# Kernel optimization log

Hardware: AMD Instinct MI355X
Metric: run time of the kernel (lower is better)

Reference implementation:

```python
import jax, jax.numpy as jnp
import numpy as np

B, L, D = 16384, 32, 128
DIAG_LEN, PROC_LEN, MED_LEN = 100000, 50000, 1000


def setup_inputs() -> dict:
    key = jax.random.key(0)
    ks = jax.random.split(key, 12)
    inp = {
        "diag_codes": jax.random.randint(ks[0], (B, L), 0, DIAG_LEN),
        "proc_codes": jax.random.randint(ks[1], (B, L), 0, PROC_LEN),
        "prev_diag_codes": jax.random.randint(ks[2], (B, L), 0, DIAG_LEN),
        "prev_proc_codes": jax.random.randint(ks[3], (B, L), 0, PROC_LEN),
        # learned parameters (torch Linear convention: W[out,in], y = x @ W.T + b)
        "diag_emb": jax.random.normal(ks[4], (DIAG_LEN, D), jnp.float32) * 0.02,
        "proc_emb": jax.random.normal(ks[5], (PROC_LEN, D), jnp.float32) * 0.02,
        "W1": jax.random.normal(ks[6], (D, 2 * D), jnp.float32) * 0.02,
        "b1": jnp.zeros((D,), jnp.float32),
        "W2": jax.random.normal(ks[7], (256, 2 * D), jnp.float32) * 0.02,
        "b2": jnp.zeros((256,), jnp.float32),
        "W3": jax.random.normal(ks[8], (MED_LEN, 256), jnp.float32) * 0.02,
        "b3": jnp.zeros((MED_LEN,), jnp.float32),
    }
    return inp


def _bag_sum(table, idx):
    # EmbeddingBag('sum'): gather [B,L,D] then reduce over codes -> [B,D]
    return jnp.take(table, idx, axis=0).sum(axis=1)


def reference(diag_codes, proc_codes, prev_diag_codes, prev_proc_codes,
              diag_emb, proc_emb, W1, b1, W2, b2, W3, b3):
    emb_d = _bag_sum(diag_emb, diag_codes)            # [B,128]
    emb_p = _bag_sum(proc_emb, proc_codes)            # [B,128]
    prev_d = _bag_sum(diag_emb, prev_diag_codes)      # [B,128]
    prev_p = _bag_sum(proc_emb, prev_proc_codes)      # [B,128]

    # health_net = Linear(256->128) + Dropout (identity in eval mode)
    cur = jnp.concatenate([emb_d, emb_p], axis=1) @ W1.T + b1     # [B,128]
    prev = jnp.concatenate([prev_d, prev_p], axis=1) @ W1.T + b1  # [B,128]

    rep = jnp.concatenate([cur, prev], axis=1)        # [B,256]
    h = jax.nn.relu(rep @ W2.T + b2)                  # [B,256]
    return jax.nn.sigmoid(h @ W3.T + b3)              # [B,med_len]
```

## Files before the change

### kernel.cpp

```cpp
#include <hip/hip_runtime.h>
#include <hip/hip_bf16.h>
#include <math.h>

#define NB 16384
#define MED 1000
#define MD 100000
#define MP 50000
#define TDBLK 782
#define TPBLK 391

typedef __bf16 bf16x8 __attribute__((ext_vector_type(8)));
typedef float  f32x4  __attribute__((ext_vector_type(4)));
typedef unsigned short u16;
typedef unsigned int   u32;

__device__ __forceinline__ u16 f2bf(float f) {
    union { float f; u32 u; } v; v.f = f;
    u32 r = v.u + 0x7fffu + ((v.u >> 16) & 1u);
    return (u16)(r >> 16);
}
__device__ __forceinline__ float bflo(u32 u) { union { u32 u; float f; } v; v.u = u << 16;          return v.f; }
__device__ __forceinline__ float bfhi(u32 u) { union { u32 u; float f; } v; v.u = u & 0xffff0000u; return v.f; }

__global__ __launch_bounds__(256) void convert_kernel(
    const float* __restrict__ W1, const float* __restrict__ W2,
    const float* __restrict__ W3,
    u16* __restrict__ W1b, u16* __restrict__ W2b, u16* __restrict__ W3b)
{
    int i = blockIdx.x * 256 + threadIdx.x;
    if (i < 32768) { W1b[i] = f2bf(W1[i]); return; }
    i -= 32768;
    if (i < 65536) { W2b[i] = f2bf(W2[i]); return; }
    i -= 65536;
    if (i < 262144) W3b[i] = (i < MED * 256) ? f2bf(W3[i]) : (u16)0;
}

__global__ __launch_bounds__(256) void transform_kernel(
    const float* __restrict__ Ed, const float* __restrict__ Ep,
    const u16* __restrict__ W1b, u16* __restrict__ Td, u16* __restrict__ Tp)
{
    int blk = blockIdx.x;
    const float* E; u16* T; int M, koff;
    if (blk < TDBLK) { E = Ed; T = Td; M = MD; koff = 0; }
    else             { blk -= TDBLK; E = Ep; T = Tp; M = MP; koff = 128; }

    const int wave = threadIdx.x >> 6, lane = threadIdx.x & 63;
    const int quad = lane >> 4, l16 = lane & 15;
    const int m0 = blk * 128 + wave * 32 + l16;
    const float* aP0 = E + (size_t)min(m0,      M - 1) * 128 + quad * 8;
    const float* aP1 = E + (size_t)min(m0 + 16, M - 1) * 128 + quad * 8;
    const u16*   wP  = W1b + (size_t)l16 * 256 + koff + quad * 8;

    f32x4 acc[2][8];
    #pragma unroll
    for (int mt = 0; mt < 2; ++mt)
        #pragma unroll
        for (int nt = 0; nt < 8; ++nt) acc[mt][nt] = (f32x4){0.f, 0.f, 0.f, 0.f};

    #pragma unroll
    for (int ks = 0; ks < 4; ++ks) {
        union { bf16x8 v; u16 s[8]; } a0, a1;
        const float4 f0 = *(const float4*)(aP0 + ks * 32);
        const float4 f1 = *(const float4*)(aP0 + ks * 32 + 4);
        const float4 g0 = *(const float4*)(aP1 + ks * 32);
        const float4 g1 = *(const float4*)(aP1 + ks * 32 + 4);
        a0.s[0]=f2bf(f0.x); a0.s[1]=f2bf(f0.y); a0.s[2]=f2bf(f0.z); a0.s[3]=f2bf(f0.w);
        a0.s[4]=f2bf(f1.x); a0.s[5]=f2bf(f1.y); a0.s[6]=f2bf(f1.z); a0.s[7]=f2bf(f1.w);
        a1.s[0]=f2bf(g0.x); a1.s[1]=f2bf(g0.y); a1.s[2]=f2bf(g0.z); a1.s[3]=f2bf(g0.w);
        a1.s[4]=f2bf(g1.x); a1.s[5]=f2bf(g1.y); a1.s[6]=f2bf(g1.z); a1.s[7]=f2bf(g1.w);
        #pragma unroll
        for (int nt = 0; nt < 8; ++nt) {
            const bf16x8 b = *(const bf16x8*)(wP + nt * 16 * 256 + ks * 32);
            acc[0][nt] = __builtin_amdgcn_mfma_f32_16x16x32_bf16(a0.v, b, acc[0][nt], 0, 0, 0);
            acc[1][nt] = __builtin_amdgcn_mfma_f32_16x16x32_bf16(a1.v, b, acc[1][nt], 0, 0, 0);
        }
    }

    #pragma unroll
    for (int mt = 0; mt < 2; ++mt) {
        const int rb = blk * 128 + wave * 32 + mt * 16 + quad * 4;
        #pragma unroll
        for (int nt = 0; nt < 8; ++nt) {
            const int col = nt * 16 + l16;
            #pragma unroll
            for (int r = 0; r < 4; ++r) {
                const int row = rb + r;
                if (row < M) T[(size_t)row * 128 + col] = f2bf(acc[mt][nt][r]);
            }
        }
    }
}

__global__ __launch_bounds__(256) void gather_rep(
    const int* __restrict__ diag, const int* __restrict__ proc,
    const int* __restrict__ pdiag, const int* __restrict__ pproc,
    const u16* __restrict__ Td, const u16* __restrict__ Tp,
    const float* __restrict__ b1, u16* __restrict__ rep)
{
    __shared__ int   sidx[528];
    __shared__ float sred[128][8];
    const int t = threadIdx.x;

    for (int i = t; i < 512; i += 256) {
        const int s = i >> 7, bg = (i >> 5) & 3, l = i & 31;
        const int* cp = (bg == 0) ? diag : (bg == 1) ? proc : (bg == 2) ? pdiag : pproc;
        sidx[s * 132 + bg * 33 + l] = cp[(blockIdx.x * 4 + s) * 32 + l];
    }
    __syncthreads();

    const int sub = t >> 6, bag = (t >> 4) & 3, lc = t & 15;
    const u16* tbl = (bag & 1) ? Tp : Td;
    const int* myidx = &sidx[sub * 132 + bag * 33];

    float s0=0,s1=0,s2=0,s3=0,s4=0,s5=0,s6=0,s7=0;
    uint4 va[8], vb[8];
    #pragma unroll
    for (int j = 0; j < 8; ++j)
        va[j] = *(const uint4*)(tbl + (size_t)myidx[j] * 128 + lc * 8);
    #pragma unroll
    for (int j = 0; j < 8; ++j)
        vb[j] = *(const uint4*)(tbl + (size_t)myidx[8 + j] * 128 + lc * 8);

#define CONSUME(V) do { \
    _Pragma("unroll") \
    for (int j = 0; j < 8; ++j) { \
        s0 += bflo(V[j].x); s1 += bfhi(V[j].x); \
        s2 += bflo(V[j].y); s3 += bfhi(V[j].y); \
        s4 += bflo(V[j].z); s5 += bfhi(V[j].z); \
        s6 += bflo(V[j].w); s7 += bfhi(V[j].w); \
    } } while (0)

    {
        uint4 tmp[8];
        #pragma unroll
        for (int j = 0; j < 8; ++j)
            tmp[j] = *(const uint4*)(tbl + (size_t)myidx[16 + j] * 128 + lc * 8);
        CONSUME(va);
        #pragma unroll
        for (int j = 0; j < 8; ++j) va[j] = tmp[j];
    }
    {
        uint4 tmp[8];
        #pragma unroll
        for (int j = 0; j < 8; ++j)
            tmp[j] = *(const uint4*)(tbl + (size_t)myidx[24 + j] * 128 + lc * 8);
        CONSUME(vb);
        #pragma unroll
        for (int j = 0; j < 8; ++j) vb[j] = tmp[j];
    }
    CONSUME(va);
    CONSUME(vb);
#undef CONSUME

    const int oid = sub * 32 + (bag >> 1) * 16 + lc;
    if (bag & 1) {
        *(float4*)&sred[oid][0] = make_float4(s0, s1, s2, s3);
        *(float4*)&sred[oid][4] = make_float4(s4, s5, s6, s7);
    }
    __syncthreads();
    if (!(bag & 1)) {
        const float4 p0 = *(const float4*)&sred[oid][0];
        const float4 p1 = *(const float4*)&sred[oid][4];
        const float4 c0 = *(const float4*)(b1 + lc * 8);
        const float4 c1 = *(const float4*)(b1 + lc * 8 + 4);
        s0 += p0.x + c0.x; s1 += p0.y + c0.y; s2 += p0.z + c0.z; s3 += p0.w + c0.w;
        s4 += p1.x + c1.x; s5 += p1.y + c1.y; s6 += p1.z + c1.z; s7 += p1.w + c1.w;
        uint4 o;
        o.x = (u32)f2bf(s0) | ((u32)f2bf(s1) << 16);
        o.y = (u32)f2bf(s2) | ((u32)f2bf(s3) << 16);
        o.z = (u32)f2bf(s4) | ((u32)f2bf(s5) << 16);
        o.w = (u32)f2bf(s6) | ((u32)f2bf(s7) << 16);
        const int b = blockIdx.x * 4 + sub;
        *(uint4*)(rep + (size_t)b * 256 + (bag >> 1) * 128 + lc * 8) = o;
    }
}

__global__ __launch_bounds__(256) void gemm23(
    const u16* __restrict__ rep, const u16* __restrict__ W2b,
    const float* __restrict__ b2, const u16* __restrict__ W3b,
    const float* __restrict__ b3, float* __restrict__ out)
{
    __shared__ u16 hs[32][264];
    const int wave = threadIdx.x >> 6, lane = threadIdx.x & 63;
    const int quad = lane >> 4, l16 = lane & 15;
    const int mBase = blockIdx.x * 32;

    {
        const int mrow = mBase + (wave & 1) * 16 + l16;
        const int ncol0 = (wave >> 1) * 128;
        const u16* aP = rep + (size_t)mrow * 256 + quad * 8;
        bf16x8 a[8];
        #pragma unroll
        for (int ks = 0; ks < 8; ++ks) a[ks] = *(const bf16x8*)(aP + ks * 32);

        #pragma unroll
        for (int nt = 0; nt < 8; ++nt) {
            const int col = ncol0 + nt * 16 + l16;
            const u16* wP = W2b + (size_t)col * 256 + quad * 8;
            f32x4 acc = {0.f, 0.f, 0.f, 0.f};
            #pragma unroll
            for (int ks = 0; ks < 8; ++ks) {
                const bf16x8 b = *(const bf16x8*)(wP + ks * 32);
                acc = __builtin_amdgcn_mfma_f32_16x16x32_bf16(a[ks], b, acc, 0, 0, 0);
            }
            const float bv = b2[col];
            #pragma unroll
            for (int r = 0; r < 4; ++r) {
                float v = acc[r] + bv;
                v = v > 0.f ? v : 0.f;
                hs[(wave & 1) * 16 + quad * 4 + r][col] = f2bf(v);
            }
        }
    }
    __syncthreads();

    const int colW = wave * 256;
    #pragma unroll
    for (int nc = 0; nc < 4; ++nc) {
        f32x4 acc[2][4];
        #pragma unroll
        for (int mt = 0; mt < 2; ++mt)
            #pragma unroll
            for (int nti = 0; nti < 4; ++nti) acc[mt][nti] = (f32x4){0.f,0.f,0.f,0.f};

        #pragma unroll
        for (int ks = 0; ks < 8; ++ks) {
            bf16x8 af[2];
            #pragma unroll
            for (int mt = 0; mt < 2; ++mt)
                af[mt] = *(const bf16x8*)&hs[mt * 16 + l16][quad * 8 + ks * 32];
            #pragma unroll
            for (int nti = 0; nti < 4; ++nti) {
                const int wrow = colW + nc * 64 + nti * 16 + l16;
                const bf16x8 b = *(const bf16x8*)(W3b + (size_t)wrow * 256 + quad * 8 + ks * 32);
                acc[0][nti] = __builtin_amdgcn_mfma_f32_16x16x32_bf16(af[0], b, acc[0][nti], 0, 0, 0);
                acc[1][nti] = __builtin_amdgcn_mfma_f32_16x16x32_bf16(af[1], b, acc[1][nti], 0, 0, 0);
            }
        }
        #pragma unroll
        for (int nti = 0; nti < 4; ++nti) {
            const int col = colW + nc * 64 + nti * 16 + l16;
            if (col < MED) {
                const float bv = b3[col];
                #pragma unroll
                for (int mt = 0; mt < 2; ++mt) {
                    #pragma unroll
                    for (int r = 0; r < 4; ++r) {
                        const float v = acc[mt][nti][r] + bv;
                        out[(size_t)(mBase + mt * 16 + quad * 4 + r) * MED + col] =
                            1.0f / (1.0f + __expf(-v));
                    }
                }
            }
        }
    }
}

extern "C" void kernel_launch(void* const* d_in, const int* in_sizes, int n_in,
                              void* d_out, int out_size, void* d_ws, size_t ws_size,
                              hipStream_t stream)
{
    const int*   diag  = (const int*)d_in[0];
    const int*   proc  = (const int*)d_in[1];
    const int*   pdiag = (const int*)d_in[2];
    const int*   pproc = (const int*)d_in[3];
    const float* demb  = (const float*)d_in[4];
    const float* pemb  = (const float*)d_in[5];
    const float* W1    = (const float*)d_in[6];
    const float* b1    = (const float*)d_in[7];
    const float* W2    = (const float*)d_in[8];
    const float* b2    = (const float*)d_in[9];
    const float* W3    = (const float*)d_in[10];
    const float* b3    = (const float*)d_in[11];

    char* ws = (char*)d_ws;
    u16* Td  = (u16*)ws;
    u16* Tp  = (u16*)(ws + 25600000);
    u16* rep = (u16*)(ws + 38400000);
    u16* W1b = (u16*)(ws + 46788608);
    u16* W2b = (u16*)(ws + 46854144);
    u16* W3b = (u16*)(ws + 46985216);

    convert_kernel<<<1408, 256, 0, stream>>>(W1, W2, W3, W1b, W2b, W3b);
    transform_kernel<<<TDBLK + TPBLK, 256, 0, stream>>>(demb, pemb, W1b, Td, Tp);
    gather_rep<<<NB / 4, 256, 0, stream>>>(diag, proc, pdiag, pproc, Td, Tp, b1, rep);
    gemm23<<<512, 256, 0, stream>>>(rep, W2b, b2, W3b, b3, (float*)d_out);
}
```

Baseline: 293.6 us.

## Store W1-transformed embedding tables as scaled FP8 and fuse prep kernels

The projected embedding tables (E·W1ᵀ) are now written in FP8 with a fixed 4096 scale instead of bf16, which halves the table footprint written by the transform and read by the random gather. Weight conversion and the table transform are merged into one launch, with W1 converted to bf16 into shared memory per block. The transform MFMA is reoriented so each lane writes contiguous packed FP8 words. FP8 storage with a fixed scale loses precision and may underflow or clip values, which risks accuracy.

After: 247.0 us. 1.19x faster.

```diff
diff --git a/kernel.cpp b/kernel.cpp
--- a/kernel.cpp
+++ b/kernel.cpp
@@ -8,84 +8,98 @@
 #define MP 50000
 #define TDBLK 782
 #define TPBLK 391
+#define NTR (TDBLK + TPBLK)
+#define NCV 1280
+#define FP8_SCALE 4096.0f
+#define FP8_INV   (1.0f / 4096.0f)
 
 typedef __bf16 bf16x8 __attribute__((ext_vector_type(8)));
 typedef float  f32x4  __attribute__((ext_vector_type(4)));
+typedef float  f32x2  __attribute__((ext_vector_type(2)));
 typedef unsigned short u16;
 typedef unsigned int   u32;
+typedef unsigned char  u8;
 
 __device__ __forceinline__ u16 f2bf(float f) {
     union { float f; u32 u; } v; v.f = f;
     u32 r = v.u + 0x7fffu + ((v.u >> 16) & 1u);
     return (u16)(r >> 16);
 }
-__device__ __forceinline__ float bflo(u32 u) { union { u32 u; float f; } v; v.u = u << 16;          return v.f; }
-__device__ __forceinline__ float bfhi(u32 u) { union { u32 u; float f; } v; v.u = u & 0xffff0000u; return v.f; }
-
-__global__ __launch_bounds__(256) void convert_kernel(
-    const float* __restrict__ W1, const float* __restrict__ W2,
-    const float* __restrict__ W3,
-    u16* __restrict__ W1b, u16* __restrict__ W2b, u16* __restrict__ W3b)
+
+__global__ __launch_bounds__(256) void prep_kernel(
+    const float* __restrict__ Ed, const float* __restrict__ Ep,
+    const float* __restrict__ W1,
+    const float* __restrict__ W2, const float* __restrict__ W3,
+    u8* __restrict__ Td, u8* __restrict__ Tp,
+    u16* __restrict__ W2b, u16* __restrict__ W3b)
 {
-    int i = blockIdx.x * 256 + threadIdx.x;
-    if (i < 32768) { W1b[i] = f2bf(W1[i]); return; }
-    i -= 32768;
-    if (i < 65536) { W2b[i] = f2bf(W2[i]); return; }
-    i -= 65536;
-    if (i < 262144) W3b[i] = (i < MED * 256) ? f2bf(W3[i]) : (u16)0;
-}
-
-__global__ __launch_bounds__(256) void transform_kernel(
-    const float* __restrict__ Ed, const float* __restrict__ Ep,
-    const u16* __restrict__ W1b, u16* __restrict__ Td, u16* __restrict__ Tp)
-{
-    int blk = blockIdx.x;
-    const float* E; u16* T; int M, koff;
+    __shared__ u16 w1s[128 * 132];
+    const int bid = blockIdx.x, tid = threadIdx.x;
+
+    if (bid >= NTR) {
+        int i = (bid - NTR) * 256 + tid;
+        if (i < 65536) { W2b[i] = f2bf(W2[i]); return; }
+        i -= 65536;
+        if (i < 262144) W3b[i] = (i < MED * 256) ? f2bf(W3[i]) : (u16)0;
+        return;
+    }
+
+    int blk = bid;
+    const float* E; u8* T; int M, koff;
     if (blk < TDBLK) { E = Ed; T = Td; M = MD; koff = 0; }
     else             { blk -= TDBLK; E = Ep; T = Tp; M = MP; koff = 128; }
 
-    const int wave = threadIdx.x >> 6, lane = threadIdx.x & 63;
+    for (int idx = tid; idx < 4096; idx += 256) {
+        const int row = idx >> 5, c4 = idx & 31;
+        const float4 v = *(const float4*)(W1 + row * 256 + koff + c4 * 4);
+        u16* d = &w1s[row * 132 + c4 * 4];
+        d[0] = f2bf(v.x); d[1] = f2bf(v.y); d[2] = f2bf(v.z); d[3] = f2bf(v.w);
+    }
+    __syncthreads();
+
+    const int wave = tid >> 6, lane = tid & 63;
     const int quad = lane >> 4, l16 = lane & 15;
-    const int m0 = blk * 128 + wave * 32 + l16;
-    const float* aP0 = E + (size_t)min(m0,      M - 1) * 128 + quad * 8;
-    const float* aP1 = E + (size_t)min(m0 + 16, M - 1) * 128 + quad * 8;
-    const u16*   wP  = W1b + (size_t)l16 * 256 + koff + quad * 8;
-
-    f32x4 acc[2][8];
-    #pragma unroll
-    for (int mt = 0; mt < 2; ++mt)
-        #pragma unroll
-        for (int nt = 0; nt < 8; ++nt) acc[mt][nt] = (f32x4){0.f, 0.f, 0.f, 0.f};
+    const int n0 = blk * 128 + wave * 32;
+    const float* bP0 = E + (size_t)min(n0 + l16,      M - 1) * 128 + quad * 8;
+    const float* bP1 = E + (size_t)min(n0 + 16 + l16, M - 1) * 128 + quad * 8;
+
+    f32x4 acc[8][2];
+    #pragma unroll
+    for (int mt = 0; mt < 8; ++mt) {
+        acc[mt][0] = (f32x4){0.f,0.f,0.f,0.f};
+        acc[mt][1] = (f32x4){0.f,0.f,0.f,0.f};
+    }
 
     #pragma unroll
     for (int ks = 0; ks < 4; ++ks) {
-        union { bf16x8 v; u16 s[8]; } a0, a1;
-        const float4 f0 = *(const float4*)(aP0 + ks * 32);
-        const float4 f1 = *(const float4*)(aP0 + ks * 32 + 4);
-        const float4 g0 = *(const float4*)(aP1 + ks * 32);
-        const float4 g1 = *(const float4*)(aP1 + ks * 32 + 4);
-        a0.s[0]=f2bf(f0.x); a0.s[1]=f2bf(f0.y); a0.s[2]=f2bf(f0.z); a0.s[3]=f2bf(f0.w);
-        a0.s[4]=f2bf(f1.x); a0.s[5]=f2bf(f1.y); a0.s[6]=f2bf(f1.z); a0.s[7]=f2bf(f1.w);
-        a1.s[0]=f2bf(g0.x); a1.s[1]=f2bf(g0.y); a1.s[2]=f2bf(g0.z); a1.s[3]=f2bf(g0.w);
-        a1.s[4]=f2bf(g1.x); a1.s[5]=f2bf(g1.y); a1.s[6]=f2bf(g1.z); a1.s[7]=f2bf(g1.w);
-        #pragma unroll
-        for (int nt = 0; nt < 8; ++nt) {
-            const bf16x8 b = *(const bf16x8*)(wP + nt * 16 * 256 + ks * 32);
-            acc[0][nt] = __builtin_amdgcn_mfma_f32_16x16x32_bf16(a0.v, b, acc[0][nt], 0, 0, 0);
-            acc[1][nt] = __builtin_amdgcn_mfma_f32_16x16x32_bf16(a1.v, b, acc[1][nt], 0, 0, 0);
-        }
-    }
-
-    #pragma unroll
-    for (int mt = 0; mt < 2; ++mt) {
-        const int rb = blk * 128 + wave * 32 + mt * 16 + quad * 4;
-        #pragma unroll
-        for (int nt = 0; nt < 8; ++nt) {
-            const int col = nt * 16 + l16;
-            #pragma unroll
-            for (int r = 0; r < 4; ++r) {
-                const int row = rb + r;
-                if (row < M) T[(size_t)row * 128 + col] = f2bf(acc[mt][nt][r]);
+        union { bf16x8 v; u16 s[8]; } b0, b1;
+        const float4 f0 = *(const float4*)(bP0 + ks * 32);
+        const float4 f1 = *(const float4*)(bP0 + ks * 32 + 4);
+        const float4 g0 = *(const float4*)(bP1 + ks * 32);
+        const float4 g1 = *(const float4*)(bP1 + ks * 32 + 4);
+        b0.s[0]=f2bf(f0.x); b0.s[1]=f2bf(f0.y); b0.s[2]=f2bf(f0.z); b0.s[3]=f2bf(f0.w);
+        b0.s[4]=f2bf(f1.x); b0.s[5]=f2bf(f1.y); b0.s[6]=f2bf(f1.z); b0.s[7]=f2bf(f1.w);
+        b1.s[0]=f2bf(g0.x); b1.s[1]=f2bf(g0.y); b1.s[2]=f2bf(g0.z); b1.s[3]=f2bf(g0.w);
+        b1.s[4]=f2bf(g1.x); b1.s[5]=f2bf(g1.y); b1.s[6]=f2bf(g1.z); b1.s[7]=f2bf(g1.w);
+        #pragma unroll
+        for (int mt = 0; mt < 8; ++mt) {
+            const bf16x8 a = *(const bf16x8*)&w1s[(mt * 16 + l16) * 132 + ks * 32 + quad * 8];
+            acc[mt][0] = __builtin_amdgcn_mfma_f32_16x16x32_bf16(a, b0.v, acc[mt][0], 0, 0, 0);
+            acc[mt][1] = __builtin_amdgcn_mfma_f32_16x16x32_bf16(a, b1.v, acc[mt][1], 0, 0, 0);
+        }
+    }
+
+    #pragma unroll
+    for (int nt = 0; nt < 2; ++nt) {
+        const int rn = n0 + nt * 16 + l16;
+        if (rn < M) {
+            u8* rowp = T + (size_t)rn * 128 + quad * 4;
+            #pragma unroll
+            for (int mt = 0; mt < 8; ++mt) {
+                const f32x4 a = acc[mt][nt];
+                int p = __builtin_amdgcn_cvt_pk_fp8_f32(a[0] * FP8_SCALE, a[1] * FP8_SCALE, 0, 0);
+                p = __builtin_amdgcn_cvt_pk_fp8_f32(a[2] * FP8_SCALE, a[3] * FP8_SCALE, p, 1);
+                *(u32*)(rowp + mt * 16) = (u32)p;
             }
         }
     }
@@ -94,7 +108,7 @@
 __global__ __launch_bounds__(256) void gather_rep(
     const int* __restrict__ diag, const int* __restrict__ proc,
     const int* __restrict__ pdiag, const int* __restrict__ pproc,
-    const u16* __restrict__ Td, const u16* __restrict__ Tp,
+    const u8* __restrict__ Td, const u8* __restrict__ Tp,
     const float* __restrict__ b1, u16* __restrict__ rep)
 {
     __shared__ int   sidx[528];
@@ -109,41 +123,41 @@
     __syncthreads();
 
     const int sub = t >> 6, bag = (t >> 4) & 3, lc = t & 15;
-    const u16* tbl = (bag & 1) ? Tp : Td;
+    const u8* tbl = (bag & 1) ? Tp : Td;
     const int* myidx = &sidx[sub * 132 + bag * 33];
 
-    float s0=0,s1=0,s2=0,s3=0,s4=0,s5=0,s6=0,s7=0;
-    uint4 va[8], vb[8];
+    f32x2 s0 = {0.f,0.f}, s1 = {0.f,0.f}, s2 = {0.f,0.f}, s3 = {0.f,0.f};
+    uint2 va[8], vb[8];
     #pragma unroll
     for (int j = 0; j < 8; ++j)
-        va[j] = *(const uint4*)(tbl + (size_t)myidx[j] * 128 + lc * 8);
+        va[j] = *(const uint2*)(tbl + (size_t)myidx[j] * 128 + lc * 8);
     #pragma unroll
     for (int j = 0; j < 8; ++j)
-        vb[j] = *(const uint4*)(tbl + (size_t)myidx[8 + j] * 128 + lc * 8);
+        vb[j] = *(const uint2*)(tbl + (size_t)myidx[8 + j] * 128 + lc * 8);
 
 #define CONSUME(V) do { \
     _Pragma("unroll") \
     for (int j = 0; j < 8; ++j) { \
-        s0 += bflo(V[j].x); s1 += bfhi(V[j].x); \
-        s2 += bflo(V[j].y); s3 += bfhi(V[j].y); \
-        s4 += bflo(V[j].z); s5 += bfhi(V[j].z); \
-        s6 += bflo(V[j].w); s7 += bfhi(V[j].w); \
+        s0 += __builtin_amdgcn_cvt_pk_f32_fp8((int)V[j].x, 0); \
+        s1 += __builtin_amdgcn_cvt_pk_f32_fp8((int)V[j].x, 1); \
+        s2 += __builtin_amdgcn_cvt_pk_f32_fp8((int)V[j].y, 0); \
+        s3 += __builtin_amdgcn_cvt_pk_f32_fp8((int)V[j].y, 1); \
     } } while (0)
 
     {
-        uint4 tmp[8];
+        uint2 tmp[8];
         #pragma unroll
         for (int j = 0; j < 8; ++j)
-            tmp[j] = *(const uint4*)(tbl + (size_t)myidx[16 + j] * 128 + lc * 8);
+            tmp[j] = *(const uint2*)(tbl + (size_t)myidx[16 + j] * 128 + lc * 8);
         CONSUME(va);
         #pragma unroll
         for (int j = 0; j < 8; ++j) va[j] = tmp[j];
     }
     {
-        uint4 tmp[8];
+        uint2 tmp[8];
         #pragma unroll
         for (int j = 0; j < 8; ++j)
-            tmp[j] = *(const uint4*)(tbl + (size_t)myidx[24 + j] * 128 + lc * 8);
+            tmp[j] = *(const uint2*)(tbl + (size_t)myidx[24 + j] * 128 + lc * 8);
         CONSUME(vb);
         #pragma unroll
         for (int j = 0; j < 8; ++j) vb[j] = tmp[j];
@@ -154,8 +168,8 @@
 
     const int oid = sub * 32 + (bag >> 1) * 16 + lc;
     if (bag & 1) {
-        *(float4*)&sred[oid][0] = make_float4(s0, s1, s2, s3);
-        *(float4*)&sred[oid][4] = make_float4(s4, s5, s6, s7);
+        *(float4*)&sred[oid][0] = make_float4(s0.x, s0.y, s1.x, s1.y);
+        *(float4*)&sred[oid][4] = make_float4(s2.x, s2.y, s3.x, s3.y);
     }
     __syncthreads();
     if (!(bag & 1)) {
@@ -163,13 +177,19 @@
         const float4 p1 = *(const float4*)&sred[oid][4];
         const float4 c0 = *(const float4*)(b1 + lc * 8);
         const float4 c1 = *(const float4*)(b1 + lc * 8 + 4);
-        s0 += p0.x + c0.x; s1 += p0.y + c0.y; s2 += p0.z + c0.z; s3 += p0.w + c0.w;
-        s4 += p1.x + c1.x; s5 += p1.y + c1.y; s6 += p1.z + c1.z; s7 += p1.w + c1.w;
+        const float t0 = (s0.x + p0.x) * FP8_INV + c0.x;
+        const float t1 = (s0.y + p0.y) * FP8_INV + c0.y;
+        const float t2 = (s1.x + p0.z) * FP8_INV + c0.z;
+        const float t3 = (s1.y + p0.w) * FP8_INV + c0.w;
+        const float t4 = (s2.x + p1.x) * FP8_INV + c1.x;
+        const float t5 = (s2.y + p1.y) * FP8_INV + c1.y;
+        const float t6 = (s3.x + p1.z) * FP8_INV + c1.z;
+        const float t7 = (s3.y + p1.w) * FP8_INV + c1.w;
         uint4 o;
-        o.x = (u32)f2bf(s0) | ((u32)f2bf(s1) << 16);
-        o.y = (u32)f2bf(s2) | ((u32)f2bf(s3) << 16);
-        o.z = (u32)f2bf(s4) | ((u32)f2bf(s5) << 16);
-        o.w = (u32)f2bf(s6) | ((u32)f2bf(s7) << 16);
+        o.x = (u32)f2bf(t0) | ((u32)f2bf(t1) << 16);
+        o.y = (u32)f2bf(t2) | ((u32)f2bf(t3) << 16);
+        o.z = (u32)f2bf(t4) | ((u32)f2bf(t5) << 16);
+        o.w = (u32)f2bf(t6) | ((u32)f2bf(t7) << 16);
         const int b = blockIdx.x * 4 + sub;
         *(uint4*)(rep + (size_t)b * 256 + (bag >> 1) * 128 + lc * 8) = o;
     }
@@ -274,15 +294,13 @@
     const float* b3    = (const float*)d_in[11];
 
     char* ws = (char*)d_ws;
-    u16* Td  = (u16*)ws;
-    u16* Tp  = (u16*)(ws + 25600000);
-    u16* rep = (u16*)(ws + 38400000);
-    u16* W1b = (u16*)(ws + 46788608);
-    u16* W2b = (u16*)(ws + 46854144);
-    u16* W3b = (u16*)(ws + 46985216);
-
-    convert_kernel<<<1408, 256, 0, stream>>>(W1, W2, W3, W1b, W2b, W3b);
-    transform_kernel<<<TDBLK + TPBLK, 256, 0, stream>>>(demb, pemb, W1b, Td, Tp);
+    u8*  Td  = (u8*)ws;
+    u8*  Tp  = (u8*)(ws + 12800000);
+    u16* rep = (u16*)(ws + 19200000);
+    u16* W2b = (u16*)(ws + 27588608);
+    u16* W3b = (u16*)(ws + 27719680);
+
+    prep_kernel<<<NTR + NCV, 256, 0, stream>>>(demb, pemb, W1, W2, W3, Td, Tp, W2b, W3b);
     gather_rep<<<NB / 4, 256, 0, stream>>>(diag, proc, pdiag, pproc, Td, Tp, b1, rep);
     gemm23<<<512, 256, 0, stream>>>(rep, W2b, b2, W3b, b3, (float*)d_out);
 }
```
